# Kernel tuning notes

Hardware: AMD Instinct MI355X
Metric: run time of the kernel (lower is better)

The kernel has to match this reference:

```python
import jax, jax.numpy as jnp
import numpy as np

B, S, E, H = 2, 2048, 1024, 16
DH = E // H  # 64


def setup_inputs() -> dict:
    key = jax.random.key(0)
    ks = jax.random.split(key, 10)
    scale = 1.0 / np.sqrt(E)
    x = jax.random.normal(ks[0], (B, S, E), dtype=jnp.float32)
    mask = jax.random.randint(ks[1], (B, S), 0, 2, dtype=jnp.int32)
    # per-head Q/K/V projections stacked: [H, E, DH] (x @ W, torch Linear transposed)
    wq = jax.random.normal(ks[2], (H, E, DH), dtype=jnp.float32) * scale
    wk = jax.random.normal(ks[3], (H, E, DH), dtype=jnp.float32) * scale
    wv = jax.random.normal(ks[4], (H, E, DH), dtype=jnp.float32) * scale
    bq = jax.random.normal(ks[5], (H, DH), dtype=jnp.float32) * scale
    bk = jax.random.normal(ks[6], (H, DH), dtype=jnp.float32) * scale
    bv = jax.random.normal(ks[7], (H, DH), dtype=jnp.float32) * scale
    wo = jax.random.normal(ks[8], (E, E), dtype=jnp.float32) * scale
    bo = jax.random.normal(ks[9], (E,), dtype=jnp.float32) * scale
    return {"x": x, "mask": mask, "wq": wq, "bq": bq, "wk": wk, "bk": bk,
            "wv": wv, "bv": bv, "wo": wo, "bo": bo}


def reference(x, mask, wq, bq, wk, bk, wv, bv, wo, bo):
    # q,k,v: [B, H, S, DH]
    q = jnp.einsum('bse,hed->bhsd', x, wq) + bq[None, :, None, :]
    k = jnp.einsum('bse,hed->bhsd', x, wk) + bk[None, :, None, :]
    v = jnp.einsum('bse,hed->bhsd', x, wv) + bv[None, :, None, :]
    scores = jnp.einsum('bhsd,bhtd->bhst', q, k) / np.sqrt(DH)
    # padding mask on key axis: mask==0 -> -1e9 (as in masked_fill)
    scores = jnp.where(mask[:, None, None, :] == 0, jnp.float32(-1e9), scores)
    attn = jax.nn.softmax(scores, axis=-1)
    o = jnp.einsum('bhst,bhtd->bhsd', attn, v)
    # concat heads -> [B, S, E], then output projection
    o = o.transpose(0, 2, 1, 3).reshape(B, S, E)
    return o @ wo + bo
```

## Files before the change

kernel.cpp:

```cpp
#include <hip/hip_runtime.h>
#include <hip/hip_bf16.h>
#include <math.h>

#define Bsz 2
#define Ssz 2048
#define Esz 1024
#define Hsz 16
#define DHsz 64

typedef __bf16 bf16_t;
typedef __attribute__((ext_vector_type(8))) __bf16 bf16x8;
typedef __attribute__((ext_vector_type(4))) float f32x4;

typedef unsigned int u32;
typedef const __attribute__((address_space(1))) u32* gptr_t;
typedef __attribute__((address_space(3))) u32* lptr_t;

#if __has_builtin(__builtin_amdgcn_exp2f)
#define EXP2F(x) __builtin_amdgcn_exp2f(x)
#else
#define EXP2F(x) __expf((x)*0.69314718f)
#endif

__device__ __forceinline__ bf16_t to_bf16(float f) {
  union { float f; unsigned u; } v; v.f = f;
  unsigned r = (v.u + 0x7FFF + ((v.u >> 16) & 1)) >> 16;
  union { unsigned short s; bf16_t b; } o; o.s = (unsigned short)r;
  return o.b;
}

__device__ __forceinline__ unsigned pack2_rtz(float a, float b) {
#if __has_builtin(__builtin_amdgcn_perm)
  return __builtin_amdgcn_perm(__float_as_uint(b), __float_as_uint(a), 0x07060302u);
#else
  return (__float_as_uint(a) >> 16) | (__float_as_uint(b) & 0xFFFF0000u);
#endif
}

__device__ __forceinline__ unsigned pack2(float a, float b) {
  union { float f; unsigned u; } x, y; x.f = a; y.f = b;
  unsigned ra = (x.u + 0x7FFF + ((x.u >> 16) & 1)) >> 16;
  unsigned rb = (y.u + 0x7FFF + ((y.u >> 16) & 1)) >> 16;
  return ra | (rb << 16);
}

__device__ __forceinline__ f32x4 mfma16(bf16x8 a, bf16x8 b, f32x4 c) {
  return __builtin_amdgcn_mfma_f32_16x16x32_bf16(a, b, c, 0, 0, 0);
}

__device__ __forceinline__ void gload16(void* lds, const void* g) {
  __builtin_amdgcn_global_load_lds((gptr_t)g, (lptr_t)lds, 16, 0, 0);
}

#define PREP_CAST 4096
#define PREP_MASK 4112
__global__ __launch_bounds__(256) void prep(
    const float* __restrict__ x, const int* __restrict__ mask,
    const float* __restrict__ wq, const float* __restrict__ wk,
    const float* __restrict__ wv, const float* __restrict__ wo,
    bf16_t* __restrict__ xb, bf16_t* __restrict__ mb,
    bf16_t* __restrict__ wAll, bf16_t* __restrict__ wAllV, bf16_t* __restrict__ woT) {
  __shared__ bf16_t lT[64 * 72];
  const int bid = blockIdx.x, t = threadIdx.x;
  if (bid < PREP_CAST) {
    const int i = bid * 256 + t;
    float4 v = ((const float4*)x)[i];
    uint2 o; o.x = pack2(v.x, v.y); o.y = pack2(v.z, v.w);
    ((uint2*)xb)[i] = o;
  } else if (bid < PREP_MASK) {
    const int i = (bid - PREP_CAST) * 256 + t;
    mb[i] = to_bf16(mask[i] ? 1.0f : 0.0f);
  } else {
    const int t2 = bid - PREP_MASK;
    const int et = t2 & 15, h = (t2 >> 4) & 15, z = t2 >> 8;
    const float* src; int srcLD; bf16_t* dst;
    if (z == 0)      { src = wq + ((size_t)h * Esz + et * 64) * DHsz; srcLD = DHsz; dst = wAll  + (size_t)(h * 64) * Esz; }
    else if (z == 1) { src = wk + ((size_t)h * Esz + et * 64) * DHsz; srcLD = DHsz; dst = wAll  + (size_t)(1024 + h * 64) * Esz; }
    else if (z == 2) { src = wv + ((size_t)h * Esz + et * 64) * DHsz; srcLD = DHsz; dst = wAllV + (size_t)(h * 64) * Esz; }
    else             { src = wo + (size_t)(et * 64) * Esz + h * 64;   srcLD = Esz;  dst = woT   + (size_t)(h * 64) * Esz; }
#pragma unroll
    for (int rr = 0; rr < 4; rr++) {
      int er = rr * 16 + (t >> 4);
      int dc = (t & 15) * 4;
      float4 v = *(const float4*)&src[(size_t)er * srcLD + dc];
      lT[(dc + 0) * 72 + er] = to_bf16(v.x);
      lT[(dc + 1) * 72 + er] = to_bf16(v.y);
      lT[(dc + 2) * 72 + er] = to_bf16(v.z);
      lT[(dc + 3) * 72 + er] = to_bf16(v.w);
    }
    __syncthreads();
#pragma unroll
    for (int rr = 0; rr < 2; rr++) {
      int d = rr * 32 + (t >> 3);
      int e8 = (t & 7) * 8;
      bf16x8 o = *(const bf16x8*)&lT[d * 72 + e8];
      *(bf16x8*)&dst[(size_t)d * Esz + et * 64 + e8] = o;
    }
  }
}

template <int TM, int TN>
__device__ __forceinline__ void gemm_core(
    const bf16_t* __restrict__ Ab, const bf16_t* __restrict__ Bb, int K,
    bf16_t* lA, bf16_t* lB, f32x4 (&acc)[TM / 32][TN / 32]) {
  const int tid = threadIdx.x, lane = tid & 63, wvi = tid >> 6;
  const int g = lane >> 4, c = lane & 15, cw = c & 7;
  const int lrow = lane >> 3, sg = lane & 7;
  const int wm = wvi >> 1, wn = wvi & 1;
  for (int kc = 0; kc < K; kc += 64) {
#pragma unroll
    for (int j = 0; j < TM / 32; j++) {
      const int base = (j * 4 + wvi) * 8;
      const int row = base + lrow;
      gload16(lA + base * 64, Ab + (size_t)row * K + kc + ((sg ^ (row & 7)) * 8));
    }
#pragma unroll
    for (int j = 0; j < TN / 32; j++) {
      const int base = (j * 4 + wvi) * 8;
      const int row = base + lrow;
      gload16(lB + base * 64, Bb + (size_t)row * K + kc + ((sg ^ (row & 7)) * 8));
    }
    __syncthreads();
#pragma unroll
    for (int ksp = 0; ksp < 2; ksp++) {
      const int kg = (ksp * 4 + g) ^ cw;
      bf16x8 af[TM / 32], bfr[TN / 32];
#pragma unroll
      for (int mt = 0; mt < TM / 32; mt++)
        af[mt] = *(const bf16x8*)&lA[(wm * (TM / 2) + mt * 16 + c) * 64 + kg * 8];
#pragma unroll
      for (int nt = 0; nt < TN / 32; nt++)
        bfr[nt] = *(const bf16x8*)&lB[(wn * (TN / 2) + nt * 16 + c) * 64 + kg * 8];
#pragma unroll
      for (int mt = 0; mt < TM / 32; mt++)
#pragma unroll
        for (int nt = 0; nt < TN / 32; nt++)
          acc[mt][nt] = mfma16(af[mt], bfr[nt], acc[mt][nt]);
    }
    __syncthreads();
  }
}

__global__ __launch_bounds__(256, 3) void qkv_gemm(
    const bf16_t* __restrict__ xb, const bf16_t* __restrict__ wAll,
    const bf16_t* __restrict__ wAllV, const bf16_t* __restrict__ mb,
    const float* __restrict__ bq, const float* __restrict__ bk,
    const float* __restrict__ bv,
    bf16_t* __restrict__ qb, bf16_t* __restrict__ kb, bf16_t* __restrict__ vTb) {
  __shared__ alignas(16) bf16_t lA[128 * 64];
  __shared__ alignas(16) bf16_t lB[128 * 64];
  const int bid = blockIdx.x;
  const int lane = threadIdx.x & 63, wvi = threadIdx.x >> 6;
  const int g = lane >> 4, c = lane & 15;
  const int wm = wvi >> 1, wn = wvi & 1;
  f32x4 acc[4][4] = {};
  if (bid < 512) {
    const int Mb = (bid & 31) * 128, Nb = (bid >> 5) * 128;
    gemm_core<128, 128>(xb + (size_t)Mb * Esz, wAll + (size_t)Nb * Esz, Esz, lA, lB, acc);
#pragma unroll
    for (int nt = 0; nt < 4; nt++) {
      const int col = Nb + wn * 64 + nt * 16 + c;
      const int which = col >> 10, h = (col >> 6) & 15, d = col & 63;
      const float bias = (which ? bk : bq)[h * DHsz + d];
      const float scale = which ? 1.0f : 0.18033688011112042f;
      bf16_t* dst = which ? kb : qb;
#pragma unroll
      for (int mt = 0; mt < 4; mt++)
#pragma unroll
        for (int r = 0; r < 4; r++) {
          const int row = Mb + wm * 64 + mt * 16 + g * 4 + r;
          const int b = row >> 11, s = row & 2047;
          dst[(((size_t)(b * Hsz + h)) * Ssz + s) * DHsz + d] =
              to_bf16((acc[mt][nt][r] + bias) * scale);
        }
    }
  } else {
    const int t2 = bid - 512;
    const int Mb = (t2 & 7) * 128, Nb = ((t2 >> 3) & 15) * 128, b = t2 >> 7;
    gemm_core<128, 128>(wAllV + (size_t)Mb * Esz, xb + ((size_t)(b * Ssz) + Nb) * Esz,
                        Esz, lA, lB, acc);
#pragma unroll
    for (int nt = 0; nt < 4; nt++) {
      const int s = Nb + wn * 64 + nt * 16 + c;
      const float mval = (float)mb[b * Ssz + s];
#pragma unroll
      for (int mt = 0; mt < 4; mt++)
#pragma unroll
        for (int r = 0; r < 4; r++) {
          const int m = Mb + wm * 64 + mt * 16 + g * 4 + r;
          vTb[((size_t)(b * 1024 + m)) * Ssz + s] = to_bf16((acc[mt][nt][r] + bv[m]) * mval);
        }
    }
  }
}

__global__ __launch_bounds__(256, 2) void flash_attn(
    const bf16_t* __restrict__ qb, const bf16_t* __restrict__ kb,
    const bf16_t* __restrict__ vTb, const bf16_t* __restrict__ mb,
    bf16_t* __restrict__ Ob) {
  __shared__ alignas(16) char smem[16384 + 4 * 2048];
  bf16_t* lK = (bf16_t*)smem;
  bf16_t* lP = (bf16_t*)(smem + 16384);
  float* cbuf = (float*)smem;

  const int h = blockIdx.x, qt = blockIdx.y, b = blockIdx.z;
  const size_t bh = (size_t)(b * Hsz + h);
  const int tid = threadIdx.x, lane = tid & 63, wv = tid >> 6;
  const int qh = wv & 1;
  const int p = wv >> 1;
  const int g = lane >> 4, c = lane & 15, cw = c & 7;
  const int lrow = lane >> 3, sg = lane & 7;
  const int smask = (c >> 1) & 7;
  const int sbase = (c >> 1) * 64 + (c & 1) * 32;

  const bf16_t* Kbase = kb + (bh * Ssz + (size_t)p * 1024) * DHsz;
  const bf16_t* Vlane = vTb + bh * (size_t)DHsz * Ssz + (size_t)c * Ssz + p * 1024 + g * 8;
  const bf16_t* mbb = mb + b * Ssz + p * 1024 + g * 8;
  bf16_t* lKp = lK + p * 2 * 2048;
  bf16_t* lPw = lP + wv * 1024;

  bf16x8 qf[2][2];
  const bf16_t* Qbase = qb + (bh * Ssz + qt * 64 + qh * 32) * DHsz;
#pragma unroll
  for (int qsub = 0; qsub < 2; qsub++)
#pragma unroll
    for (int ksp = 0; ksp < 2; ksp++)
      qf[qsub][ksp] = *(const bf16x8*)&Qbase[(qsub * 16 + c) * DHsz + ksp * 32 + g * 8];

  f32x4 o[2][4] = {};
  f32x4 lac[2] = {};

  auto stage = [&](int tc, int buf) {
#pragma unroll
    for (int j = 0; j < 2; j++) {
      const int rowbase = qh * 16 + j * 8;
      const int row = rowbase + lrow;
      gload16(&lKp[buf * 2048 + rowbase * 64],
              Kbase + ((size_t)(tc * 32 + row)) * DHsz + (sg ^ lrow) * 8);
    }
  };

  auto loadVM = [&](int tc, bf16x8 (&vf)[4], bf16x8& mfr) {
    const bf16_t* vp = Vlane + tc * 32;
    mfr = *(const bf16x8*)&mbb[tc * 32];
#pragma unroll
    for (int dt = 0; dt < 4; dt++)
      vf[dt] = *(const bf16x8*)&vp[dt * 16 * Ssz];
  };

  auto compute = [&](int buf, bf16x8 (&vf)[4], bf16x8& mfr) {
    const bf16_t* Kt = lKp + buf * 2048;
    f32x4 st[2][2] = {};
#pragma unroll
    for (int ksp = 0; ksp < 2; ksp++) {
      const int kgr = (ksp * 4 + g) ^ cw;
#pragma unroll
      for (int nt = 0; nt < 2; nt++) {
        bf16x8 kf = *(const bf16x8*)&Kt[(nt * 16 + c) * 64 + kgr * 8];
        st[0][nt] = mfma16(kf, qf[0][ksp], st[0][nt]);
        st[1][nt] = mfma16(kf, qf[1][ksp], st[1][nt]);
      }
    }
#pragma unroll
    for (int qsub = 0; qsub < 2; qsub++)
#pragma unroll
      for (int nt = 0; nt < 2; nt++) {
        float p0 = EXP2F(st[qsub][nt][0]);
        float p1 = EXP2F(st[qsub][nt][1]);
        float p2 = EXP2F(st[qsub][nt][2]);
        float p3 = EXP2F(st[qsub][nt][3]);
        const int slot = (((c & 1) * 4) + nt * 2 + (g >> 1)) ^ smask;
        uint2 pv; pv.x = pack2_rtz(p0, p1); pv.y = pack2_rtz(p2, p3);
        *(uint2*)&lPw[qsub * 512 + (c >> 1) * 64 + slot * 8 + (g & 1) * 4] = pv;
      }
    const int slotr = (((c & 1) * 4) + g) ^ smask;
    bf16x8 pf0 = *(const bf16x8*)&lPw[0 * 512 + (c >> 1) * 64 + slotr * 8];
    bf16x8 pf1 = *(const bf16x8*)&lPw[1 * 512 + (c >> 1) * 64 + slotr * 8];
    lac[0] = mfma16(pf0, mfr, lac[0]);
    lac[1] = mfma16(pf1, mfr, lac[1]);
#pragma unroll
    for (int dt = 0; dt < 4; dt++) {
      o[0][dt] = mfma16(pf0, vf[dt], o[0][dt]);
      o[1][dt] = mfma16(pf1, vf[dt], o[1][dt]);
    }
  };

  bf16x8 vA[4], vB[4], mA, mB;
  stage(0, 0);
  loadVM(0, vA, mA);
  __syncthreads();
  for (int tc = 0; tc < 32; tc += 2) {
    stage(tc + 1, 1);
    loadVM(tc + 1, vB, mB);
    compute(0, vA, mA);
    __syncthreads();
    if (tc + 2 < 32) {
      stage(tc + 2, 0);
      loadVM(tc + 2, vA, mA);
    }
    compute(1, vB, mB);
    __syncthreads();
  }

  if (p == 1) {
    float* cb = cbuf + ((size_t)(qh * 64 + lane)) * 40;
#pragma unroll
    for (int qsub = 0; qsub < 2; qsub++)
#pragma unroll
      for (int dt = 0; dt < 4; dt++)
        *(f32x4*)&cb[(qsub * 4 + dt) * 4] = o[qsub][dt];
    *(f32x4*)&cb[32] = lac[0];
    *(f32x4*)&cb[36] = lac[1];
  }
  __syncthreads();
  if (p == 0) {
    const float* cb = cbuf + ((size_t)(qh * 64 + lane)) * 40;
#pragma unroll
    for (int qsub = 0; qsub < 2; qsub++)
#pragma unroll
      for (int dt = 0; dt < 4; dt++)
        o[qsub][dt] += *(const f32x4*)&cb[(qsub * 4 + dt) * 4];
    lac[0] += *(const f32x4*)&cb[32];
    lac[1] += *(const f32x4*)&cb[36];

#pragma unroll
    for (int qsub = 0; qsub < 2; qsub++)
#pragma unroll
      for (int r = 0; r < 4; r++) {
        const int row = qsub * 16 + g * 4 + r;
        const float linv = 1.0f / fmaxf(lac[qsub][r], 1e-30f);
        const size_t orow = (size_t)(b * Ssz + qt * 64 + qh * 32 + row) * Esz + h * DHsz;
#pragma unroll
        for (int dt = 0; dt < 4; dt++)
          Ob[orow + dt * 16 + c] = to_bf16(o[qsub][dt][r] * linv);
      }
  }
}

__global__ __launch_bounds__(256, 3) void out_gemm(
    const bf16_t* __restrict__ Ob, const bf16_t* __restrict__ woT,
    const float* __restrict__ bo, float* __restrict__ out) {
  __shared__ alignas(16) bf16_t lA[128 * 64];
  __shared__ alignas(16) bf16_t lB[64 * 64];
  f32x4 acc[4][2] = {};
  const int Mb = blockIdx.x * 128, Nb = blockIdx.y * 64;
  gemm_core<128, 64>(Ob + (size_t)Mb * Esz, woT + (size_t)Nb * Esz, Esz, lA, lB, acc);
  const int lane = threadIdx.x & 63, wvi = threadIdx.x >> 6;
  const int g = lane >> 4, c = lane & 15;
  const int wm = wvi >> 1, wn = wvi & 1;
#pragma unroll
  for (int nt = 0; nt < 2; nt++) {
    const int col = Nb + wn * 32 + nt * 16 + c;
    const float bias = bo[col];
#pragma unroll
    for (int mt = 0; mt < 4; mt++)
#pragma unroll
      for (int r = 0; r < 4; r++) {
        const int row = Mb + wm * 64 + mt * 16 + g * 4 + r;
        out[(size_t)row * Esz + col] = acc[mt][nt][r] + bias;
      }
  }
}

extern "C" void kernel_launch(void* const* d_in, const int* in_sizes, int n_in,
                              void* d_out, int out_size, void* d_ws, size_t ws_size,
                              hipStream_t stream) {
  const float* x = (const float*)d_in[0];
  const int* mask = (const int*)d_in[1];
  const float* wq = (const float*)d_in[2];
  const float* bq = (const float*)d_in[3];
  const float* wk = (const float*)d_in[4];
  const float* bk = (const float*)d_in[5];
  const float* wv = (const float*)d_in[6];
  const float* bv = (const float*)d_in[7];
  const float* wo = (const float*)d_in[8];
  const float* bo = (const float*)d_in[9];
  float* out = (float*)d_out;

  char* ws = (char*)d_ws;
  size_t off = 0;
  auto take = [&](size_t bytes) -> char* {
    char* p = ws + off;
    off += (bytes + 255) & ~(size_t)255;
    return p;
  };
  bf16_t* xb    = (bf16_t*)take((size_t)Bsz * Ssz * Esz * 2);
  bf16_t* wAll  = (bf16_t*)take((size_t)2 * Esz * Esz * 2);
  bf16_t* wAllV = (bf16_t*)take((size_t)Esz * Esz * 2);
  bf16_t* woT   = (bf16_t*)take((size_t)Esz * Esz * 2);
  bf16_t* qb    = (bf16_t*)take((size_t)Bsz * Hsz * Ssz * DHsz * 2);
  bf16_t* kb    = (bf16_t*)take((size_t)Bsz * Hsz * Ssz * DHsz * 2);
  bf16_t* vTb   = (bf16_t*)take((size_t)Bsz * Hsz * Ssz * DHsz * 2);
  bf16_t* Ob    = (bf16_t*)take((size_t)Bsz * Ssz * Esz * 2);
  bf16_t* mb    = (bf16_t*)take((size_t)Bsz * Ssz * 2);

  prep<<<5136, 256, 0, stream>>>(x, mask, wq, wk, wv, wo, xb, mb, wAll, wAllV, woT);
  qkv_gemm<<<768, 256, 0, stream>>>(xb, wAll, wAllV, mb, bq, bk, bv, qb, kb, vTb);
  flash_attn<<<dim3(Hsz, Ssz / 64, Bsz), 256, 0, stream>>>(qb, kb, vTb, mb, Ob);
  out_gemm<<<dim3(Bsz * Ssz / 128, Esz / 64), 256, 0, stream>>>(Ob, woT, bo, out);
}
```

Measured before the change: 222.9 us.

## Load K fragments directly into registers and drop LDS staging and barriers

K tiles are now read straight from global memory into per-lane MFMA fragment registers, with double buffering in registers, instead of being staged into swizzled shared memory. This removes the per-iteration __syncthreads barriers and LDS traffic for K, and shrinks shared memory to the reduction buffer. The cost is extra register pressure and global reads of K duplicated across the two waves that share the same key half, now relying on cache instead of LDS reuse. The loop is also kept rolled (unroll 1) with a peeled tail.

```diff
diff --git a/kernel.cpp b/kernel.cpp
--- a/kernel.cpp
+++ b/kernel.cpp
@@ -198,9 +198,8 @@
     const bf16_t* __restrict__ qb, const bf16_t* __restrict__ kb,
     const bf16_t* __restrict__ vTb, const bf16_t* __restrict__ mb,
     bf16_t* __restrict__ Ob) {
-  __shared__ alignas(16) char smem[16384 + 4 * 2048];
-  bf16_t* lK = (bf16_t*)smem;
-  bf16_t* lP = (bf16_t*)(smem + 16384);
+  __shared__ alignas(16) char smem[2 * 64 * 40 * 4];
+  bf16_t* lP = (bf16_t*)smem;
   float* cbuf = (float*)smem;
 
   const int h = blockIdx.x, qt = blockIdx.y, b = blockIdx.z;
@@ -208,15 +207,13 @@
   const int tid = threadIdx.x, lane = tid & 63, wv = tid >> 6;
   const int qh = wv & 1;
   const int p = wv >> 1;
-  const int g = lane >> 4, c = lane & 15, cw = c & 7;
-  const int lrow = lane >> 3, sg = lane & 7;
+  const int g = lane >> 4, c = lane & 15;
   const int smask = (c >> 1) & 7;
-  const int sbase = (c >> 1) * 64 + (c & 1) * 32;
 
   const bf16_t* Kbase = kb + (bh * Ssz + (size_t)p * 1024) * DHsz;
+  const bf16_t* Klane = Kbase + (size_t)c * DHsz + g * 8;
   const bf16_t* Vlane = vTb + bh * (size_t)DHsz * Ssz + (size_t)c * Ssz + p * 1024 + g * 8;
   const bf16_t* mbb = mb + b * Ssz + p * 1024 + g * 8;
-  bf16_t* lKp = lK + p * 2 * 2048;
   bf16_t* lPw = lP + wv * 1024;
 
   bf16x8 qf[2][2];
@@ -230,14 +227,13 @@
   f32x4 o[2][4] = {};
   f32x4 lac[2] = {};
 
-  auto stage = [&](int tc, int buf) {
-#pragma unroll
-    for (int j = 0; j < 2; j++) {
-      const int rowbase = qh * 16 + j * 8;
-      const int row = rowbase + lrow;
-      gload16(&lKp[buf * 2048 + rowbase * 64],
-              Kbase + ((size_t)(tc * 32 + row)) * DHsz + (sg ^ lrow) * 8);
-    }
+  auto loadK = [&](int tc, bf16x8 (&kf)[2][2]) {
+    const bf16_t* kp = Klane + (size_t)tc * 32 * DHsz;
+#pragma unroll
+    for (int ksp = 0; ksp < 2; ksp++)
+#pragma unroll
+      for (int nt = 0; nt < 2; nt++)
+        kf[ksp][nt] = *(const bf16x8*)&kp[(size_t)nt * 16 * DHsz + ksp * 32];
   };
 
   auto loadVM = [&](int tc, bf16x8 (&vf)[4], bf16x8& mfr) {
@@ -248,19 +244,15 @@
       vf[dt] = *(const bf16x8*)&vp[dt * 16 * Ssz];
   };
 
-  auto compute = [&](int buf, bf16x8 (&vf)[4], bf16x8& mfr) {
-    const bf16_t* Kt = lKp + buf * 2048;
+  auto compute = [&](bf16x8 (&kf)[2][2], bf16x8 (&vf)[4], bf16x8& mfr) {
     f32x4 st[2][2] = {};
 #pragma unroll
-    for (int ksp = 0; ksp < 2; ksp++) {
-      const int kgr = (ksp * 4 + g) ^ cw;
+    for (int ksp = 0; ksp < 2; ksp++)
 #pragma unroll
       for (int nt = 0; nt < 2; nt++) {
-        bf16x8 kf = *(const bf16x8*)&Kt[(nt * 16 + c) * 64 + kgr * 8];
-        st[0][nt] = mfma16(kf, qf[0][ksp], st[0][nt]);
-        st[1][nt] = mfma16(kf, qf[1][ksp], st[1][nt]);
+        st[0][nt] = mfma16(kf[ksp][nt], qf[0][ksp], st[0][nt]);
+        st[1][nt] = mfma16(kf[ksp][nt], qf[1][ksp], st[1][nt]);
       }
-    }
 #pragma unroll
     for (int qsub = 0; qsub < 2; qsub++)
 #pragma unroll
@@ -285,23 +277,20 @@
     }
   };
 
-  bf16x8 vA[4], vB[4], mA, mB;
-  stage(0, 0);
-  loadVM(0, vA, mA);
+  bf16x8 kA[2][2], kB[2][2], vA[4], vB[4], mA, mB;
+  loadK(0, kA); loadVM(0, vA, mA);
+  loadK(1, kB); loadVM(1, vB, mB);
+#pragma unroll 1
+  for (int tc = 0; tc < 30; tc += 2) {
+    compute(kA, vA, mA);
+    loadK(tc + 2, kA); loadVM(tc + 2, vA, mA);
+    compute(kB, vB, mB);
+    loadK(tc + 3, kB); loadVM(tc + 3, vB, mB);
+  }
+  compute(kA, vA, mA);
+  compute(kB, vB, mB);
+
   __syncthreads();
-  for (int tc = 0; tc < 32; tc += 2) {
-    stage(tc + 1, 1);
-    loadVM(tc + 1, vB, mB);
-    compute(0, vA, mA);
-    __syncthreads();
-    if (tc + 2 < 32) {
-      stage(tc + 2, 0);
-      loadVM(tc + 2, vA, mA);
-    }
-    compute(1, vB, mB);
-    __syncthreads();
-  }
-
   if (p == 1) {
     float* cb = cbuf + ((size_t)(qh * 64 + lane)) * 40;
 #pragma unroll
```

New measurement: 269.8 us. 1.21x slower.
